# Optimization experiments

Hardware: AMD Instinct MI355X
Metric: run time of the kernel (lower is better)

## Reference

```python
import jax, jax.numpy as jnp
import numpy as np


def conv2d(x, w, b, pad):
    y = jax.lax.conv_general_dilated(x, w, (1, 1), [(pad, pad), (pad, pad)],
                                     dimension_numbers=('NCHW', 'OIHW', 'NCHW'))
    return y + b[None, :, None, None]


def setup_inputs() -> dict:
    key = jax.random.key(0)
    ks = jax.random.split(key, 24)
    bs, C, OC, K = 2, 64, 3, 3
    hi = wi = 96
    ho = wo = 192

    def _w(k, o, i, kh, kw):
        return jax.random.normal(k, (o, i, kh, kw), jnp.float32) / np.float32(np.sqrt(i * kh * kw))

    inp = {
        'x': jax.random.normal(ks[0], (bs, C, hi, wi), jnp.float32),
        'poseMap': jax.random.normal(ks[1], (1, 3, ho, wo), jnp.float32),
        'interMapY': jax.random.randint(ks[2], (ho, wo), 0, hi, jnp.int32),
        'interMapX': jax.random.randint(ks[3], (ho, wo), 0, wi, jnp.int32),
        # sigmaconv: 3x3 convs 64->64->64->2
        'sig_w1': _w(ks[4], 64, 64, 3, 3), 'sig_b1': jnp.zeros((64,), jnp.float32),
        'sig_w2': _w(ks[5], 64, 64, 3, 3), 'sig_b2': jnp.zeros((64,), jnp.float32),
        'sig_w3': _w(ks[6], 2, 64, 3, 3), 'sig_b3': jnp.zeros((2,), jnp.float32),
        # dwconv: 1x1 convs 3->64->256->C*K*K
        'dw_w1': _w(ks[7], 64, 3, 1, 1), 'dw_b1': jnp.zeros((64,), jnp.float32),
        'dw_w2': _w(ks[8], 256, 64, 1, 1), 'dw_b2': jnp.zeros((256,), jnp.float32),
        'dw_w3': _w(ks[9], C * K * K, 256, 1, 1), 'dw_b3': jnp.zeros((C * K * K,), jnp.float32),
        # pwconv: 1x1 convs 3->64->256->C*OC
        'pw_w1': _w(ks[10], 64, 3, 1, 1), 'pw_b1': jnp.zeros((64,), jnp.float32),
        'pw_w2': _w(ks[11], 256, 64, 1, 1), 'pw_b2': jnp.zeros((256,), jnp.float32),
        'pw_w3': _w(ks[12], C * OC, 256, 1, 1), 'pw_b3': jnp.zeros((C * OC,), jnp.float32),
    }
    return inp


def reference(x, poseMap, interMapY, interMapX,
              sig_w1, sig_b1, sig_w2, sig_b2, sig_w3, sig_b3,
              dw_w1, dw_b1, dw_w2, dw_b2, dw_w3, dw_b3,
              pw_w1, pw_b1, pw_w2, pw_b2, pw_w3, pw_b3):
    C, K, OC = 64, 3, 3
    bs, _, hi, wi = x.shape
    ho, wo = poseMap.shape[2], poseMap.shape[3]
    pad = K // 2

    p = jax.lax.stop_gradient(poseMap)  # original detaches poseMap
    # kernel-predict branches (1x1 conv MLPs over position map)
    dw = conv2d(jax.nn.relu(conv2d(jax.nn.relu(conv2d(p, dw_w1, dw_b1, 0)), dw_w2, dw_b2, 0)), dw_w3, dw_b3, 0)
    dw = dw.reshape(1, C, K * K, ho, wo)
    pw = conv2d(jax.nn.relu(conv2d(jax.nn.relu(conv2d(p, pw_w1, pw_b1, 0)), pw_w2, pw_b2, 0)), pw_w3, pw_b3, 0)
    pw = pw.reshape(C, OC, ho, wo)

    # unfold(x, K, padding=K//2): [bs, C, K*K, hi, wi], kernel taps row-major
    xp = jnp.pad(x, ((0, 0), (0, 0), (pad, pad), (pad, pad)))
    h = jnp.stack([xp[:, :, dy:dy + hi, dx:dx + wi]
                   for dy in range(K) for dx in range(K)], axis=2)
    # irregular spatial gather to HR grid: [bs, C, K*K, ho, wo]
    h = h[:, :, :, interMapY, interMapX]

    mean = jnp.sum(h * jax.nn.softmax(dw, axis=2), axis=2)  # [bs, C, ho, wo]
    sigma = conv2d(jax.nn.relu(conv2d(jax.nn.relu(conv2d(mean, sig_w1, sig_b1, 1)), sig_w2, sig_b2, 1)), sig_w3, sig_b3, 1)
    sigmad = sigma[:, 0:1, None, :, :]
    sigmar = sigma[:, 1:2, None, :, :]
    bw = sigmad * dw + sigmar * jnp.abs(h - mean[:, :, None, :, :])
    xa = jnp.sum(h * jax.nn.softmax(bw, axis=2), axis=2)  # [bs, C, ho, wo]
    out = jnp.einsum('bchw,cohw->bohw', xa, pw)  # [bs, OC, ho, wo]
    return out
```

## Files before the change

### kernel.cpp

```cpp
#include <hip/hip_runtime.h>
#include <hip/hip_bf16.h>

#define NPIX 36864

typedef __attribute__((ext_vector_type(8))) short short8;
typedef __attribute__((ext_vector_type(4))) short short4v;
typedef __attribute__((ext_vector_type(4))) float float4v;

__device__ inline unsigned short f2b(float x) {
    return __builtin_bit_cast(unsigned short, __float2bfloat16(x));
}
__device__ inline float b2f(unsigned short h) {
    return __uint_as_float(((unsigned int)h) << 16);
}

#define WB_TOTAL 312320
#define XCAST_N  1179648
__global__ __launch_bounds__(256) void prep_all(
    const float* __restrict__ dw2, const float* __restrict__ dw3,
    const float* __restrict__ pw2, const float* __restrict__ pw3,
    const float* __restrict__ sw1, const float* __restrict__ sw2,
    const float* __restrict__ sw3, unsigned short* __restrict__ wb,
    const float* __restrict__ x, unsigned short* __restrict__ xb)
{
    int i = blockIdx.x * 256 + threadIdx.x;
    if (i >= WB_TOTAL) {
        int j = i - WB_TOTAL;
        if (j < XCAST_N) xb[j] = f2b(x[j]);
        return;
    }
    unsigned short v;
    if (i < 16384)        v = f2b(dw2[i]);
    else if (i < 32768)   v = f2b(pw2[i - 16384]);
    else if (i < 180224)  v = f2b(dw3[i - 32768]);
    else if (i < 229376)  v = f2b(pw3[i - 180224]);
    else if (i < 266240) { int j = i - 229376; int t = j / 4096, r = j % 4096, oc = r / 64, ic = r % 64;
                           v = f2b(sw1[(oc * 64 + ic) * 9 + t]); }
    else if (i < 303104) { int j = i - 266240; int t = j / 4096, r = j % 4096, oc = r / 64, ic = r % 64;
                           v = f2b(sw2[(oc * 64 + ic) * 9 + t]); }
    else                 { int j = i - 303104; int t = j / 1024, r = j % 1024, oc = r / 64, ic = r % 64;
                           v = (oc < 2) ? f2b(sw3[(oc * 64 + ic) * 9 + t]) : (unsigned short)0; }
    wb[i] = v;
}

__global__ __launch_bounds__(512, 2) void mlp_fused(
    const float* __restrict__ pose,
    const float* __restrict__ w1A, const float* __restrict__ b1A,
    const float* __restrict__ w1B, const float* __restrict__ b1B,
    const unsigned short* __restrict__ w2A, const unsigned short* __restrict__ w2B,
    const float* __restrict__ b2A, const float* __restrict__ b2B,
    const unsigned short* __restrict__ w33,
    const float* __restrict__ b3A, const float* __restrict__ b3B,
    unsigned short* __restrict__ outA, unsigned short* __restrict__ outB)
{
    __shared__ unsigned short sh[65536];
    unsigned short* Ws  = sh;
    unsigned short* h2s = sh + 49152;
    unsigned short* h1s = h2s;
    unsigned short* Ts  = h2s;
    const int tid = threadIdx.x;
    const int u = blockIdx.y;
    const int chain = (u == 3) ? 1 : 0;
    const int w = tid >> 6, l = tid & 63;
    const int ln = l & 15, lkg = l >> 4, lk = lkg * 8;
    const float* w1 = chain ? w1B : w1A;
    const float* b1 = chain ? b1B : b1A;
    const unsigned short* w2 = chain ? w2B : w2A;
    const float* b2 = chain ? b2B : b2A;
    const int rowbase = chain ? 576 : u * 192;
    const int obase   = chain ? 0 : u * 192;
    const float* b3 = chain ? b3B : b3A;
    unsigned short* outp = chain ? outB : outA;

    for (int i = 0; i < 12; ++i) {
        const int chunk = (i * 8 + w) * 1024;
        int a  = chunk + l * 16;
        int ap = a ^ (((a >> 9) & 7) << 4);
        const unsigned short* gp =
            &w33[(size_t)(rowbase + (ap >> 9)) * 256 + ((ap & 511) >> 1)];
        __builtin_amdgcn_global_load_lds(
            (const __attribute__((address_space(1))) void*)gp,
            (__attribute__((address_space(3))) void*)((char*)Ws + chunk),
            16, 0, 0);
    }
    short8 Aw2[2][2];
    #pragma unroll
    for (int mt = 0; mt < 2; ++mt) {
        int ocr = w * 32 + mt * 16 + ln;
        Aw2[mt][0] = *(const short8*)&w2[(size_t)ocr * 64 + lk];
        Aw2[mt][1] = *(const short8*)&w2[(size_t)ocr * 64 + 32 + lk];
    }
    const int nh = w & 1, mb = w >> 1;
    const int pxbase = blockIdx.x * 576;
    float p0 = pose[pxbase + l], p1 = pose[NPIX + pxbase + l], p2 = pose[2 * NPIX + pxbase + l];

    for (int it = 0; it < 9; ++it) {
        const int px0 = pxbase + it * 64;
        {
            short8 s0;
            #pragma unroll
            for (int j = 0; j < 8; ++j) {
                int oc = w * 8 + j;
                float v = b1[oc] + w1[oc * 3] * p0 + w1[oc * 3 + 1] * p1 + w1[oc * 3 + 2] * p2;
                s0[j] = (short)f2b(fmaxf(v, 0.f));
            }
            *(short8*)&h1s[w * 512 + l * 8] = s0;
        }
        float np0 = 0.f, np1 = 0.f, np2 = 0.f;
        if (it < 8) {
            int pxn = px0 + 64 + l;
            np0 = pose[pxn]; np1 = pose[NPIX + pxn]; np2 = pose[2 * NPIX + pxn];
        }
        __syncthreads();
        short8 b0v[4], b1v[4];
        #pragma unroll
        for (int nt = 0; nt < 4; ++nt) {
            b0v[nt] = *(const short8*)&h1s[(lkg    ) * 512 + (nt * 16 + ln) * 8];
            b1v[nt] = *(const short8*)&h1s[(4 + lkg) * 512 + (nt * 16 + ln) * 8];
        }
        __syncthreads();
        {
            float4v acc2[2][4] = {};
            #pragma unroll
            for (int mt = 0; mt < 2; ++mt) {
                #pragma unroll
                for (int nt = 0; nt < 4; ++nt) {
                    acc2[mt][nt] = __builtin_amdgcn_mfma_f32_16x16x32_bf16(Aw2[mt][0], b0v[nt], acc2[mt][nt], 0, 0, 0);
                    acc2[mt][nt] = __builtin_amdgcn_mfma_f32_16x16x32_bf16(Aw2[mt][1], b1v[nt], acc2[mt][nt], 0, 0, 0);
                }
            }
            #pragma unroll
            for (int mt = 0; mt < 2; ++mt) {
                int ocb = w * 32 + mt * 16 + lkg * 4;
                int chk = ocb >> 3, pos = (lkg & 1) * 4;
                float bv0 = b2[ocb + 0], bv1 = b2[ocb + 1], bv2 = b2[ocb + 2], bv3 = b2[ocb + 3];
                #pragma unroll
                for (int nt = 0; nt < 4; ++nt) {
                    int pxl = nt * 16 + ln;
                    short4v pk;
                    pk[0] = (short)f2b(fmaxf(acc2[mt][nt][0] + bv0, 0.f));
                    pk[1] = (short)f2b(fmaxf(acc2[mt][nt][1] + bv1, 0.f));
                    pk[2] = (short)f2b(fmaxf(acc2[mt][nt][2] + bv2, 0.f));
                    pk[3] = (short)f2b(fmaxf(acc2[mt][nt][3] + bv3, 0.f));
                    *(short4v*)&h2s[chk * 512 + pxl * 8 + pos] = pk;
                }
            }
        }
        __syncthreads();
        float4v acc[3][2] = {};
        {
            const int r0l = mb * 16 + ln;
            const int swz = (r0l & 7) << 4;
            const char* Wb = (const char*)Ws;
            #pragma unroll
            for (int kc = 0; kc < 8; ++kc) {
                short8 a0 = *(const short8*)(Wb + (((r0l      ) * 512 + kc * 64 + lk * 2) ^ swz));
                short8 a1 = *(const short8*)(Wb + (((r0l +  64) * 512 + kc * 64 + lk * 2) ^ swz));
                short8 a2 = *(const short8*)(Wb + (((r0l + 128) * 512 + kc * 64 + lk * 2) ^ swz));
                #pragma unroll
                for (int ni = 0; ni < 2; ++ni) {
                    int nt = nh * 2 + ni;
                    short8 b = *(const short8*)&h2s[(kc * 4 + lkg) * 512 + (nt * 16 + ln) * 8];
                    acc[0][ni] = __builtin_amdgcn_mfma_f32_16x16x32_bf16(a0, b, acc[0][ni], 0, 0, 0);
                    acc[1][ni] = __builtin_amdgcn_mfma_f32_16x16x32_bf16(a1, b, acc[1][ni], 0, 0, 0);
                    acc[2][ni] = __builtin_amdgcn_mfma_f32_16x16x32_bf16(a2, b, acc[2][ni], 0, 0, 0);
                }
            }
        }
        __syncthreads();
        #pragma unroll
        for (int s = 0; s < 3; ++s) {
            const int tr = (mb + s * 4) * 16 + lkg * 4;
            #pragma unroll
            for (int r = 0; r < 4; ++r) {
                float bv = b3[obase + tr + r];
                #pragma unroll
                for (int ni = 0; ni < 2; ++ni) {
                    int nt = nh * 2 + ni;
                    Ts[(tr + r) * 72 + nt * 16 + ln] = f2b(acc[s][ni][r] + bv);
                }
            }
        }
        __syncthreads();
        for (int i = tid; i < 1536; i += 512) {
            int row = i >> 3, pc = (i & 7) * 8;
            *(short8*)&outp[(size_t)(obase + row) * NPIX + px0 + pc] = *(const short8*)&Ts[row * 72 + pc];
        }
        __syncthreads();
        p0 = np0; p1 = np1; p2 = np2;
    }
}

template<int MT>
__global__ __launch_bounds__(256) void conv3x3_mfma(
    const unsigned short* __restrict__ act, const unsigned short* __restrict__ wgt,
    const float* __restrict__ bias, unsigned short* __restrict__ out,
    int relu)
{
    constexpr int SP = 72;
    constexpr int OCP = MT * 16;
    __shared__ unsigned short Bs[4 * 66 * SP];
    const int tid = threadIdx.x;
    int bx = blockIdx.x;
    const int xt = bx % 3; bx /= 3;
    const int yg = bx % 96; const int b = bx / 96;
    const int y0 = yg * 2;
    const int x0 = xt * 64;
    const size_t actb = (size_t)b * NPIX * 64;
    const int w = tid >> 6, l = tid & 63;
    const int ln = l & 15, lkg = l >> 4, lk = lkg * 8;
    const int mt = (MT == 4) ? w : 0;
    short8 Wr[9][2];
    #pragma unroll
    for (int t = 0; t < 9; ++t)
        #pragma unroll
        for (int hh = 0; hh < 2; ++hh)
            Wr[t][hh] = *(const short8*)&wgt[((size_t)t * OCP + mt * 16 + ln) * 64 + hh * 32 + lk];
    for (int s = tid; s < 264; s += 256) {
        int r = s / 66, i = s % 66;
        int yy = y0 + r - 1, xx = x0 + i - 1;
        unsigned short* dst = &Bs[(r * 66 + i) * SP];
        if (yy >= 0 && yy < 192 && xx >= 0 && xx < 192) {
            const unsigned short* src = &act[actb + (size_t)(yy * 192 + xx) * 64];
            #pragma unroll
            for (int j = 0; j < 8; ++j) *(short8*)(dst + j * 8) = *(const short8*)(src + j * 8);
        } else {
            short8 z = {};
            #pragma unroll
            for (int j = 0; j < 8; ++j) *(short8*)(dst + j * 8) = z;
        }
    }
    __syncthreads();
    const int NT = (MT == 4) ? 4 : 1;
    const int ntb = (MT == 4) ? 0 : w;
    float4v acc[2][4] = {};
    #pragma unroll
    for (int t = 0; t < 9; ++t) {
        const int r = t / 3, dx = t % 3;
        #pragma unroll
        for (int hh = 0; hh < 2; ++hh) {
            #pragma unroll
            for (int o = 0; o < 2; ++o) {
                #pragma unroll
                for (int n = 0; n < 4; ++n) {
                    if (n >= NT) break;
                    int slot = (o + r) * 66 + (ntb + n) * 16 + ln + dx;
                    short8 bf = *(const short8*)&Bs[slot * SP + hh * 32 + lk];
                    acc[o][n] = __builtin_amdgcn_mfma_f32_16x16x32_bf16(Wr[t][hh], bf, acc[o][n], 0, 0, 0);
                }
            }
        }
    }
    #pragma unroll
    for (int o = 0; o < 2; ++o) {
        #pragma unroll
        for (int n = 0; n < 4; ++n) {
            if (n >= NT) break;
            int px = (y0 + o) * 192 + x0 + (ntb + n) * 16 + ln;
            if (MT == 4) {
                int oc = mt * 16 + lkg * 4;
                float v0 = acc[o][n][0] + bias[oc + 0];
                float v1 = acc[o][n][1] + bias[oc + 1];
                float v2 = acc[o][n][2] + bias[oc + 2];
                float v3 = acc[o][n][3] + bias[oc + 3];
                if (relu) { v0 = fmaxf(v0, 0.f); v1 = fmaxf(v1, 0.f); v2 = fmaxf(v2, 0.f); v3 = fmaxf(v3, 0.f); }
                uint2 pk;
                pk.x = (unsigned int)f2b(v0) | (((unsigned int)f2b(v1)) << 16);
                pk.y = (unsigned int)f2b(v2) | (((unsigned int)f2b(v3)) << 16);
                *(uint2*)&out[((size_t)b * NPIX + px) * 64 + oc] = pk;
            } else if (lkg == 0) {
                float v0 = acc[o][n][0] + bias[0];
                float v1 = acc[o][n][1] + bias[1];
                out[((size_t)b * 2 + 0) * NPIX + px] = f2b(v0);
                out[((size_t)b * 2 + 1) * NPIX + px] = f2b(v1);
            }
        }
    }
}

#define PLSZ 10192
__global__ __launch_bounds__(256) void mean_k(
    const unsigned short* __restrict__ xb, const int* __restrict__ imy, const int* __restrict__ imx,
    const unsigned short* __restrict__ dw, unsigned short* __restrict__ mean_cm)
{
    __shared__ unsigned short pl[PLSZ];
    const int c = blockIdx.y;
    const int px0 = blockIdx.x * 1024;
    const int tid = threadIdx.x;
    {
        short8 z = {};
        short8* pf = (short8*)pl;
        for (int i = tid; i < PLSZ / 8; i += 256) pf[i] = z;
    }
    float wk[4][9];
    int base[4];
    #pragma unroll
    for (int q = 0; q < 4; ++q) {
        int px = px0 + q * 256 + tid;
        base[q] = imy[px] * 104 + imx[px] + 3;
        float d[9];
        #pragma unroll
        for (int k = 0; k < 9; ++k) d[k] = b2f(dw[(size_t)(c * 9 + k) * NPIX + px]);
        float m = d[0];
        #pragma unroll
        for (int k = 1; k < 9; ++k) m = fmaxf(m, d[k]);
        float s = 0.f;
        #pragma unroll
        for (int k = 0; k < 9; ++k) { wk[q][k] = __expf(d[k] - m); s += wk[q][k]; }
        float inv = 1.f / s;
        #pragma unroll
        for (int k = 0; k < 9; ++k) wk[q][k] *= inv;
    }
    #pragma unroll
    for (int b = 0; b < 2; ++b) {
        __syncthreads();
        const unsigned short* xp = xb + (size_t)(b * 64 + c) * 9216;
        for (int i = tid; i < 96 * 12; i += 256) {
            int row = i / 12, ch = i % 12;
            const short4v* src = (const short4v*)&xp[row * 96 + ch * 8];
            unsigned short* dd = &pl[(row + 1) * 104 + 4 + ch * 8];
            *(short4v*)dd = src[0];
            *(short4v*)(dd + 4) = src[1];
        }
        __syncthreads();
        #pragma unroll
        for (int q = 0; q < 4; ++q) {
            int px = px0 + q * 256 + tid;
            float a = 0.f;
            #pragma unroll
            for (int k = 0; k < 9; ++k)
                a += wk[q][k] * b2f(pl[base[q] + (k / 3) * 104 + (k % 3)]);
            mean_cm[(size_t)(b * 64 + c) * NPIX + px] = f2b(a);
        }
    }
}

__global__ __launch_bounds__(256) void tr_k(
    const unsigned short* __restrict__ in, unsigned short* __restrict__ out)
{
    __shared__ unsigned short T[64 * 68];
    int px0 = blockIdx.x * 64;
    int b = blockIdx.y;
    int tid = threadIdx.x;
    for (int i = tid; i < 4096; i += 256) {
        int c = i >> 6, p = i & 63;
        T[p * 68 + c] = in[(size_t)(b * 64 + c) * NPIX + px0 + p];
    }
    __syncthreads();
    for (int i = tid; i < 4096; i += 256) {
        int p = i >> 6, c = i & 63;
        out[((size_t)b * NPIX + px0 + p) * 64 + c] = T[p * 68 + c];
    }
}

__global__ __launch_bounds__(256) void xa_k(
    const unsigned short* __restrict__ xb, const int* __restrict__ imy, const int* __restrict__ imx,
    const unsigned short* __restrict__ dw, const unsigned short* __restrict__ mean_cm,
    const unsigned short* __restrict__ sigma, unsigned short* __restrict__ xab)
{
    __shared__ unsigned short pl[PLSZ];
    const int c = blockIdx.y;
    const int px0 = blockIdx.x * 1024;
    const int tid = threadIdx.x;
    {
        short8 z = {};
        short8* pf = (short8*)pl;
        for (int i = tid; i < PLSZ / 8; i += 256) pf[i] = z;
    }
    float d[4][9];
    int base[4];
    #pragma unroll
    for (int q = 0; q < 4; ++q) {
        int px = px0 + q * 256 + tid;
        base[q] = imy[px] * 104 + imx[px] + 3;
        #pragma unroll
        for (int k = 0; k < 9; ++k) d[q][k] = b2f(dw[(size_t)(c * 9 + k) * NPIX + px]);
    }
    #pragma unroll
    for (int b = 0; b < 2; ++b) {
        __syncthreads();
        const unsigned short* xp = xb + (size_t)(b * 64 + c) * 9216;
        for (int i = tid; i < 96 * 12; i += 256) {
            int row = i / 12, ch = i % 12;
            const short4v* src = (const short4v*)&xp[row * 96 + ch * 8];
            unsigned short* dd = &pl[(row + 1) * 104 + 4 + ch * 8];
            *(short4v*)dd = src[0];
            *(short4v*)(dd + 4) = src[1];
        }
        __syncthreads();
        #pragma unroll
        for (int q = 0; q < 4; ++q) {
            int px = px0 + q * 256 + tid;
            float mn = b2f(mean_cm[(size_t)(b * 64 + c) * NPIX + px]);
            float sd = b2f(sigma[((size_t)b * 2 + 0) * NPIX + px]);
            float sr = b2f(sigma[((size_t)b * 2 + 1) * NPIX + px]);
            float h[9], bw[9];
            #pragma unroll
            for (int k = 0; k < 9; ++k) {
                h[k] = b2f(pl[base[q] + (k / 3) * 104 + (k % 3)]);
                bw[k] = sd * d[q][k] + sr * fabsf(h[k] - mn);
            }
            float m = bw[0];
            #pragma unroll
            for (int k = 1; k < 9; ++k) m = fmaxf(m, bw[k]);
            float s = 0.f, a = 0.f;
            #pragma unroll
            for (int k = 0; k < 9; ++k) { float e = __expf(bw[k] - m); s += e; a += e * h[k]; }
            xab[(size_t)(b * 64 + c) * NPIX + px] = f2b(a / s);
        }
    }
}

__global__ __launch_bounds__(256) void einsum_k(
    const unsigned short* __restrict__ xab, const unsigned short* __restrict__ pw,
    float* __restrict__ out)
{
    __shared__ float red[3][4][64];
    const int tid = threadIdx.x;
    const int pxl = tid & 63, cq = tid >> 6;
    const int px = blockIdx.x * 64 + pxl;
    const int b = blockIdx.y;
    float a0 = 0.f, a1 = 0.f, a2 = 0.f;
    #pragma unroll
    for (int ci = 0; ci < 16; ++ci) {
        int c = cq * 16 + ci;
        float v = b2f(xab[(size_t)(b * 64 + c) * NPIX + px]);
        a0 += v * b2f(pw[(size_t)(c * 3 + 0) * NPIX + px]);
        a1 += v * b2f(pw[(size_t)(c * 3 + 1) * NPIX + px]);
        a2 += v * b2f(pw[(size_t)(c * 3 + 2) * NPIX + px]);
    }
    red[0][cq][pxl] = a0;
    red[1][cq][pxl] = a1;
    red[2][cq][pxl] = a2;
    __syncthreads();
    if (cq < 3) {
        float s = red[cq][0][pxl] + red[cq][1][pxl] + red[cq][2][pxl] + red[cq][3][pxl];
        out[((size_t)b * 3 + cq) * NPIX + px] = s;
    }
}

extern "C" void kernel_launch(void* const* d_in, const int* in_sizes, int n_in,
                              void* d_out, int out_size, void* d_ws, size_t ws_size,
                              hipStream_t stream)
{
    (void)in_sizes; (void)n_in; (void)out_size; (void)ws_size;
    const float* x      = (const float*)d_in[0];
    const float* pose   = (const float*)d_in[1];
    const int*   imy    = (const int*)d_in[2];
    const int*   imx    = (const int*)d_in[3];
    const float* sig_w1 = (const float*)d_in[4];
    const float* sig_b1 = (const float*)d_in[5];
    const float* sig_w2 = (const float*)d_in[6];
    const float* sig_b2 = (const float*)d_in[7];
    const float* sig_w3 = (const float*)d_in[8];
    const float* sig_b3 = (const float*)d_in[9];
    const float* dw_w1  = (const float*)d_in[10];
    const float* dw_b1  = (const float*)d_in[11];
    const float* dw_w2  = (const float*)d_in[12];
    const float* dw_b2  = (const float*)d_in[13];
    const float* dw_w3  = (const float*)d_in[14];
    const float* dw_b3  = (const float*)d_in[15];
    const float* pw_w1  = (const float*)d_in[16];
    const float* pw_b1  = (const float*)d_in[17];
    const float* pw_w2  = (const float*)d_in[18];
    const float* pw_b2  = (const float*)d_in[19];
    const float* pw_w3  = (const float*)d_in[20];
    const float* pw_b3  = (const float*)d_in[21];
    float* out = (float*)d_out;

    unsigned short* ws = (unsigned short*)d_ws;
    size_t off = 0;
    unsigned short* wb      = ws + off; off += WB_TOTAL;
    unsigned short* xb16    = ws + off; off += (size_t)XCAST_N;
    unsigned short* dwbuf   = ws + off; off += (size_t)576 * NPIX;
    unsigned short* pwbuf   = ws + off; off += (size_t)192 * NPIX;
    unsigned short* mean_cm = ws + off; off += (size_t)2 * 64 * NPIX;
    unsigned short* mean_pm = ws + off; off += (size_t)2 * NPIX * 64;
    unsigned short* s1      = ws + off; off += (size_t)2 * NPIX * 64;
    unsigned short* s2      = ws + off; off += (size_t)2 * NPIX * 64;
    unsigned short* sigma   = ws + off; off += (size_t)2 * 2 * NPIX;
    unsigned short* xab     = ws + off; off += (size_t)2 * 64 * NPIX;

    unsigned short* w_dw2 = wb + 0;
    unsigned short* w_pw2 = wb + 16384;
    unsigned short* w_33  = wb + 32768;
    unsigned short* w_s1t = wb + 229376;
    unsigned short* w_s2t = wb + 266240;
    unsigned short* w_s3t = wb + 303104;

    dim3 blk(256);
    prep_all<<<dim3((WB_TOTAL + XCAST_N + 255) / 256), blk, 0, stream>>>(
        dw_w2, dw_w3, pw_w2, pw_w3, sig_w1, sig_w2, sig_w3, wb, x, xb16);
    mlp_fused<<<dim3(64, 4), dim3(512), 0, stream>>>(
        pose, dw_w1, dw_b1, pw_w1, pw_b1, w_dw2, w_pw2, dw_b2, pw_b2,
        w_33, dw_b3, pw_b3, dwbuf, pwbuf);
    mean_k<<<dim3(36, 64), blk, 0, stream>>>(xb16, imy, imx, dwbuf, mean_cm);
    tr_k<<<dim3(576, 2), blk, 0, stream>>>(mean_cm, mean_pm);
    conv3x3_mfma<4><<<dim3(576), blk, 0, stream>>>(mean_pm, w_s1t, sig_b1, s1, 1);
    conv3x3_mfma<4><<<dim3(576), blk, 0, stream>>>(s1,      w_s2t, sig_b2, s2, 1);
    conv3x3_mfma<1><<<dim3(576), blk, 0, stream>>>(s2,      w_s3t, sig_b3, sigma, 0);
    xa_k<<<dim3(36, 64), blk, 0, stream>>>(xb16, imy, imx, dwbuf, mean_cm, sigma, xab);
    einsum_k<<<dim3(576, 2), blk, 0, stream>>>(xab, pwbuf, out);
}
```

Measured before the change: 231.1 us.

## Remove LDS staging and barriers in fused MLP, hoist bias and weight loads

Gives the layer-1 activations their own LDS region so they no longer alias the layer-2 buffer, which lets two block-wide barriers per iteration go. The LDS staging of the output tile is dropped: results are written straight from the MFMA accumulators to global memory as 2-byte stores, removing two more barriers. Layer-1 weights and the biases for all three layers are loaded once into registers before the loop instead of every iteration. In exchange, LDS use grows and the output stores become narrow and less coalesced, and holding the hoisted values raises register pressure.

```diff
diff --git a/kernel.cpp b/kernel.cpp
--- a/kernel.cpp
+++ b/kernel.cpp
@@ -53,11 +53,10 @@
     const float* __restrict__ b3A, const float* __restrict__ b3B,
     unsigned short* __restrict__ outA, unsigned short* __restrict__ outB)
 {
-    __shared__ unsigned short sh[65536];
+    __shared__ unsigned short sh[69632];
     unsigned short* Ws  = sh;
     unsigned short* h2s = sh + 49152;
-    unsigned short* h1s = h2s;
-    unsigned short* Ts  = h2s;
+    unsigned short* h1s = sh + 65536;
     const int tid = threadIdx.x;
     const int u = blockIdx.y;
     const int chain = (u == 3) ? 1 : 0;
@@ -90,7 +89,28 @@
         Aw2[mt][0] = *(const short8*)&w2[(size_t)ocr * 64 + lk];
         Aw2[mt][1] = *(const short8*)&w2[(size_t)ocr * 64 + 32 + lk];
     }
+    float w1r[8][3], b1r[8];
+    #pragma unroll
+    for (int j = 0; j < 8; ++j) {
+        int oc = w * 8 + j;
+        w1r[j][0] = w1[oc * 3]; w1r[j][1] = w1[oc * 3 + 1]; w1r[j][2] = w1[oc * 3 + 2];
+        b1r[j] = b1[oc];
+    }
+    float b2r[2][4];
+    #pragma unroll
+    for (int mt = 0; mt < 2; ++mt) {
+        int ocb = w * 32 + mt * 16 + lkg * 4;
+        #pragma unroll
+        for (int r = 0; r < 4; ++r) b2r[mt][r] = b2[ocb + r];
+    }
     const int nh = w & 1, mb = w >> 1;
+    float b3r[3][4];
+    #pragma unroll
+    for (int s = 0; s < 3; ++s) {
+        int tr0 = (mb + s * 4) * 16 + lkg * 4;
+        #pragma unroll
+        for (int r = 0; r < 4; ++r) b3r[s][r] = b3[obase + tr0 + r];
+    }
     const int pxbase = blockIdx.x * 576;
     float p0 = pose[pxbase + l], p1 = pose[NPIX + pxbase + l], p2 = pose[2 * NPIX + pxbase + l];
 
@@ -100,8 +120,7 @@
             short8 s0;
             #pragma unroll
             for (int j = 0; j < 8; ++j) {
-                int oc = w * 8 + j;
-                float v = b1[oc] + w1[oc * 3] * p0 + w1[oc * 3 + 1] * p1 + w1[oc * 3 + 2] * p2;
+                float v = b1r[j] + w1r[j][0] * p0 + w1r[j][1] * p1 + w1r[j][2] * p2;
                 s0[j] = (short)f2b(fmaxf(v, 0.f));
             }
             *(short8*)&h1s[w * 512 + l * 8] = s0;
@@ -112,14 +131,13 @@
             np0 = pose[pxn]; np1 = pose[NPIX + pxn]; np2 = pose[2 * NPIX + pxn];
         }
         __syncthreads();
-        short8 b0v[4], b1v[4];
-        #pragma unroll
-        for (int nt = 0; nt < 4; ++nt) {
-            b0v[nt] = *(const short8*)&h1s[(lkg    ) * 512 + (nt * 16 + ln) * 8];
-            b1v[nt] = *(const short8*)&h1s[(4 + lkg) * 512 + (nt * 16 + ln) * 8];
-        }
-        __syncthreads();
         {
+            short8 b0v[4], b1v[4];
+            #pragma unroll
+            for (int nt = 0; nt < 4; ++nt) {
+                b0v[nt] = *(const short8*)&h1s[(lkg    ) * 512 + (nt * 16 + ln) * 8];
+                b1v[nt] = *(const short8*)&h1s[(4 + lkg) * 512 + (nt * 16 + ln) * 8];
+            }
             float4v acc2[2][4] = {};
             #pragma unroll
             for (int mt = 0; mt < 2; ++mt) {
@@ -133,15 +151,14 @@
             for (int mt = 0; mt < 2; ++mt) {
                 int ocb = w * 32 + mt * 16 + lkg * 4;
                 int chk = ocb >> 3, pos = (lkg & 1) * 4;
-                float bv0 = b2[ocb + 0], bv1 = b2[ocb + 1], bv2 = b2[ocb + 2], bv3 = b2[ocb + 3];
                 #pragma unroll
                 for (int nt = 0; nt < 4; ++nt) {
                     int pxl = nt * 16 + ln;
                     short4v pk;
-                    pk[0] = (short)f2b(fmaxf(acc2[mt][nt][0] + bv0, 0.f));
-                    pk[1] = (short)f2b(fmaxf(acc2[mt][nt][1] + bv1, 0.f));
-                    pk[2] = (short)f2b(fmaxf(acc2[mt][nt][2] + bv2, 0.f));
-                    pk[3] = (short)f2b(fmaxf(acc2[mt][nt][3] + bv3, 0.f));
+                    pk[0] = (short)f2b(fmaxf(acc2[mt][nt][0] + b2r[mt][0], 0.f));
+                    pk[1] = (short)f2b(fmaxf(acc2[mt][nt][1] + b2r[mt][1], 0.f));
+                    pk[2] = (short)f2b(fmaxf(acc2[mt][nt][2] + b2r[mt][2], 0.f));
+                    pk[3] = (short)f2b(fmaxf(acc2[mt][nt][3] + b2r[mt][3], 0.f));
                     *(short4v*)&h2s[chk * 512 + pxl * 8 + pos] = pk;
                 }
             }
@@ -167,26 +184,19 @@
                 }
             }
         }
-        __syncthreads();
         #pragma unroll
         for (int s = 0; s < 3; ++s) {
-            const int tr = (mb + s * 4) * 16 + lkg * 4;
+            const int tr0 = (mb + s * 4) * 16 + lkg * 4;
             #pragma unroll
             for (int r = 0; r < 4; ++r) {
-                float bv = b3[obase + tr + r];
+                const size_t rowoff = (size_t)(obase + tr0 + r) * NPIX + px0;
                 #pragma unroll
                 for (int ni = 0; ni < 2; ++ni) {
-                    int nt = nh * 2 + ni;
-                    Ts[(tr + r) * 72 + nt * 16 + ln] = f2b(acc[s][ni][r] + bv);
+                    int px = nh * 32 + ni * 16 + ln;
+                    outp[rowoff + px] = f2b(acc[s][ni][r] + b3r[s][r]);
                 }
             }
         }
-        __syncthreads();
-        for (int i = tid; i < 1536; i += 512) {
-            int row = i >> 3, pc = (i & 7) * 8;
-            *(short8*)&outp[(size_t)(obase + row) * NPIX + px0 + pc] = *(const short8*)&Ts[row * 72 + pc];
-        }
-        __syncthreads();
         p0 = np0; p1 = np1; p2 = np2;
     }
 }
```

New measurement: 232.4 us. No clear change (+0.6%).
